# Performance work log

Measured on AMD Instinct MI355X. Metric: run time of the kernel, lower is better.

## Reference

```python
import jax, jax.numpy as jnp
import numpy as np

B, S, D, H = 2, 2048, 1024, 16
DK = D // H


def setup_inputs() -> dict:
    key = jax.random.key(0)
    ks = jax.random.split(key, 11)
    s = 1.0 / np.sqrt(D)
    inp = {
        "q": jax.random.normal(ks[0], (B, S, D), jnp.float32),
        "k": jax.random.normal(ks[1], (B, S, D), jnp.float32),
        "v": jax.random.normal(ks[2], (B, S, D), jnp.float32),
        "mask": jnp.tril(jnp.ones((S, S), jnp.int32))[None, None],  # [1,1,S,S] causal
        "wq": jax.random.normal(ks[3], (D, D), jnp.float32) * s,
        "bq": jax.random.normal(ks[4], (D,), jnp.float32) * s,
        "wk": jax.random.normal(ks[5], (D, D), jnp.float32) * s,
        "bk": jax.random.normal(ks[6], (D,), jnp.float32) * s,
        "wv": jax.random.normal(ks[7], (D, D), jnp.float32) * s,
        "bv": jax.random.normal(ks[8], (D,), jnp.float32) * s,
        "wo": jax.random.normal(ks[9], (D, D), jnp.float32) * s,
        "bo": jax.random.normal(ks[10], (D,), jnp.float32) * s,
    }
    return inp


def reference(q, k, v, mask, wq, bq, wk, bk, wv, bv, wo, bo):
    # Linear projections (torch Linear: x @ W.T + b)
    def split_heads(x):  # [B,S,D] -> [B,H,S,DK]
        return x.reshape(B, S, H, DK).transpose(0, 2, 1, 3)

    query = split_heads(q @ wq.T + bq)
    key_ = split_heads(k @ wk.T + bk)
    value = split_heads(v @ wv.T + bv)

    scale = 1.0 / jnp.sqrt(jnp.asarray(DK, q.dtype))
    scores = jnp.einsum("bhqd,bhkd->bhqk", query, key_) * scale
    scores = jnp.where(mask == 0, jnp.asarray(-1e9, scores.dtype), scores)
    attn = jax.nn.softmax(scores, axis=-1)  # dropout=0.0 -> identity
    x = jnp.einsum("bhqk,bhkd->bhqd", attn, value)
    x = x.transpose(0, 2, 1, 3).reshape(B, S, D)
    return x @ wo.T + bo
```

## Files before the change

kernel.cpp:

```cpp
#include <hip/hip_runtime.h>

typedef unsigned short u16;
typedef __bf16 bf16x8 __attribute__((ext_vector_type(8)));
typedef u16 u16x8 __attribute__((ext_vector_type(8)));
typedef float f32x4 __attribute__((ext_vector_type(4)));

constexpr size_t WQo = 12582912;
constexpr size_t WOo = 15728640;
constexpr size_t QPo = 16777216;
constexpr size_t KPo = 20971520;
constexpr size_t VTo = 25165824;
constexpr size_t OOo = 29360128;

#define GLD(g, l) __builtin_amdgcn_global_load_lds( \
    (const __attribute__((address_space(1))) void*)(g), \
    (__attribute__((address_space(3))) void*)(l), 16, 0, 0)

__device__ __forceinline__ u16 f2bf(float f) {
  unsigned u = __builtin_bit_cast(unsigned, f);
  u += 0x7fffu + ((u >> 16) & 1u);
  return (u16)(u >> 16);
}

__device__ __forceinline__ f32x4 zero4() {
  f32x4 z = {0.f, 0.f, 0.f, 0.f};
  return z;
}

__device__ __forceinline__ f32x4 mfma16(u16x8 a, u16x8 b, f32x4 c) {
  return __builtin_amdgcn_mfma_f32_16x16x32_bf16(
      __builtin_bit_cast(bf16x8, a), __builtin_bit_cast(bf16x8, b), c, 0, 0, 0);
}

__global__ __launch_bounds__(256) void cast_all(
    const float4* __restrict__ q, const float4* __restrict__ k, const float4* __restrict__ v,
    const float4* __restrict__ wq, const float4* __restrict__ wk,
    const float4* __restrict__ wv, const float4* __restrict__ wo,
    ushort4* __restrict__ dst)
{
  int i = blockIdx.x * 256 + threadIdx.x;
  constexpr int QN = 1048576;
  constexpr int WN = 262144;
  float4 val;
  if (i < QN)            val = q[i];
  else if (i < 2 * QN)   val = k[i - QN];
  else if (i < 3 * QN)   val = v[i - 2 * QN];
  else {
    int j = i - 3 * QN;
    if (j < WN)          val = wq[j];
    else if (j < 2 * WN) val = wk[j - WN];
    else if (j < 3 * WN) val = wv[j - 2 * WN];
    else                 val = wo[j - 3 * WN];
  }
  ushort4 o;
  o.x = f2bf(val.x); o.y = f2bf(val.y); o.z = f2bf(val.z); o.w = f2bf(val.w);
  dst[i] = o;
}

__device__ __forceinline__ void gemm_core(
    const u16* __restrict__ A, const u16* __restrict__ W,
    const float* __restrict__ bias, void* __restrict__ outp, int mode)
{
  constexpr int Kd = 1024;
  __shared__ u16 As[128 * 32];
  __shared__ u16 Bs[128 * 32];
  const int tid = threadIdx.x;
  const int wave = tid >> 6, lane = tid & 63;
  const int q4 = lane >> 4, l15 = lane & 15;
  const int m0 = blockIdx.y * 128, n0 = blockIdx.x * 128;
  const int wm = (wave >> 1) * 64, wn = (wave & 1) * 64;

  f32x4 acc[4][4];
#pragma unroll
  for (int i = 0; i < 4; ++i)
#pragma unroll
    for (int j = 0; j < 4; ++j) acc[i][j] = zero4();

  const int ch0 = wave * 128 + lane;
  const int ch1 = ch0 + 64;
  const int ra0 = ch0 >> 2, ka0 = (ch0 & 3) * 8;
  const int ra1 = ch1 >> 2, ka1 = (ch1 & 3) * 8;

  for (int kt = 0; kt < Kd; kt += 32) {
    GLD(A + (size_t)(m0 + ra0) * Kd + kt + ka0, As + wave * 1024);
    GLD(A + (size_t)(m0 + ra1) * Kd + kt + ka1, As + wave * 1024 + 512);
    GLD(W + (size_t)(n0 + ra0) * Kd + kt + ka0, Bs + wave * 1024);
    GLD(W + (size_t)(n0 + ra1) * Kd + kt + ka1, Bs + wave * 1024 + 512);
    __syncthreads();
    u16x8 af[4], bfv[4];
#pragma unroll
    for (int i = 0; i < 4; ++i)
      af[i] = *(const u16x8*)&As[(wm + i * 16 + l15) * 32 + q4 * 8];
#pragma unroll
    for (int j = 0; j < 4; ++j)
      bfv[j] = *(const u16x8*)&Bs[(wn + j * 16 + l15) * 32 + q4 * 8];
#pragma unroll
    for (int i = 0; i < 4; ++i)
#pragma unroll
      for (int j = 0; j < 4; ++j)
        acc[i][j] = mfma16(af[i], bfv[j], acc[i][j]);
    __syncthreads();
  }

#pragma unroll
  for (int i = 0; i < 4; ++i) {
    const int mb = m0 + wm + i * 16 + q4 * 4;
#pragma unroll
    for (int j = 0; j < 4; ++j) {
      const int col = n0 + wn + j * 16 + l15;
      const float bsv = bias[col];
#pragma unroll
      for (int r = 0; r < 4; ++r) {
        const float val = acc[i][j][r] + bsv;
        const int m = mb + r;
        if (mode == 0) {
          const int bb = m >> 11, s = m & 2047, hh = col >> 6, dk = col & 63;
          ((u16*)outp)[((size_t)(bb * 16 + hh) * 2048 + s) * 64 + dk] = f2bf(val);
        } else if (mode == 1) {
          const int bb = m >> 11, s = m & 2047, hh = col >> 6, dk = col & 63;
          ((u16*)outp)[((size_t)(bb * 16 + hh) * 64 + dk) * 2048 + s] = f2bf(val);
        } else {
          ((float*)outp)[(size_t)m * 1024 + col] = val;
        }
      }
    }
  }
}

__global__ __launch_bounds__(256) void proj_gemm(
    u16* __restrict__ ws, const float* __restrict__ bq,
    const float* __restrict__ bk, const float* __restrict__ bv)
{
  const int z = blockIdx.z;
  const u16* A = ws + (size_t)z * 4194304;
  const u16* W = ws + WQo + (size_t)z * 1048576;
  const float* bias = (z == 0) ? bq : ((z == 1) ? bk : bv);
  u16* outp = ws + QPo + (size_t)z * 4194304;
  gemm_core(A, W, bias, outp, (z == 2) ? 1 : 0);
}

__global__ __launch_bounds__(256) void out_gemm(
    const u16* __restrict__ ws, const float* __restrict__ bo, float* __restrict__ out)
{
  gemm_core(ws + OOo, ws + WOo, bo, out, 3);
}

__global__ __launch_bounds__(256) void flash_attn(u16* __restrict__ ws)
{
  constexpr int S = 2048;
  const int a = blockIdx.x;
  const int b = 31 - blockIdx.x;
  const int bh = blockIdx.y;
  const int bb = bh >> 4, h = bh & 15;
  const int tid = threadIdx.x;
  const int wave = tid >> 6, lane = tid & 63;
  const int q4 = lane >> 4, l15 = lane & 15;

  __shared__ u16 QsA[64 * 64];
  __shared__ u16 QsB[64 * 64];
  __shared__ u16 Ks[2][64 * 64];
  __shared__ u16 Vs[2][64 * 64];

  const u16* Qg = ws + QPo + (size_t)bh * S * 64;
  const u16* Kg = ws + KPo + (size_t)bh * S * 64;
  const u16* Vg = ws + VTo + (size_t)bh * 64 * S;
  u16* Og = ws + OOo;

  const int ch0 = wave * 128 + lane;
  const int ch1 = ch0 + 64;
  const int r0 = ch0 >> 3, c0 = (ch0 & 7) ^ (r0 & 7);
  const int r1 = ch1 >> 3, c1 = (ch1 & 7) ^ (r1 & 7);

  GLD(Qg + (size_t)(a * 64 + r0) * 64 + c0 * 8, QsA + wave * 1024);
  GLD(Qg + (size_t)(a * 64 + r1) * 64 + c1 * 8, QsA + wave * 1024 + 512);
  GLD(Qg + (size_t)(b * 64 + r0) * 64 + c0 * 8, QsB + wave * 1024);
  GLD(Qg + (size_t)(b * 64 + r1) * 64 + c1 * 8, QsB + wave * 1024 + 512);
  GLD(Kg + (size_t)r0 * 64 + c0 * 8, Ks[0] + wave * 1024);
  GLD(Kg + (size_t)r1 * 64 + c1 * 8, Ks[0] + wave * 1024 + 512);
  GLD(Vg + (size_t)r0 * S + c0 * 8, Vs[0] + wave * 1024);
  GLD(Vg + (size_t)r1 * S + c1 * 8, Vs[0] + wave * 1024 + 512);
  __syncthreads();

  u16x8 qfA[2], qfB[2];
  {
    const int row = wave * 16 + l15;
#pragma unroll
    for (int kk = 0; kk < 2; ++kk) {
      const int c = (kk * 4 + q4) ^ (row & 7);
      qfA[kk] = *(const u16x8*)&QsA[row * 64 + c * 8];
      qfB[kk] = *(const u16x8*)&QsB[row * 64 + c * 8];
    }
  }
  u16* Ps = QsA + wave * 1024;

  f32x4 oA[4], oB[4];
  float lA[4], lB[4];
#pragma unroll
  for (int j = 0; j < 4; ++j) { oA[j] = zero4(); oB[j] = zero4(); }
#pragma unroll
  for (int r = 0; r < 4; ++r) { lA[r] = 0.f; lB[r] = 0.f; }

  for (int kt = 0; kt <= b; ++kt) {
    const u16* Ksb = Ks[kt & 1];
    const u16* Vsb = Vs[kt & 1];
    if (kt < b) {
      const u16* Kt = Kg + (size_t)(kt + 1) * 64 * 64;
      u16* Kd = Ks[(kt + 1) & 1];
      u16* Vd = Vs[(kt + 1) & 1];
      GLD(Kt + (size_t)r0 * 64 + c0 * 8, Kd + wave * 1024);
      GLD(Kt + (size_t)r1 * 64 + c1 * 8, Kd + wave * 1024 + 512);
      GLD(Vg + (size_t)r0 * S + (kt + 1) * 64 + c0 * 8, Vd + wave * 1024);
      GLD(Vg + (size_t)r1 * S + (kt + 1) * 64 + c1 * 8, Vd + wave * 1024 + 512);
    }

    auto process = [&](const u16x8* qf, f32x4* o_acc, float* l_p, int qt, bool diag) {
      f32x4 sf[4];
#pragma unroll
      for (int j = 0; j < 4; ++j) {
        f32x4 z = zero4();
        const int row = j * 16 + l15;
#pragma unroll
        for (int kk = 0; kk < 2; ++kk) {
          const int c = (kk * 4 + q4) ^ (row & 7);
          z = mfma16(qf[kk], *(const u16x8*)&Ksb[row * 64 + c * 8], z);
        }
        sf[j] = z;
      }
      if (diag) {
        const int rowg0 = qt * 64 + wave * 16 + q4 * 4;
#pragma unroll
        for (int j = 0; j < 4; ++j) {
          const int colg = kt * 64 + j * 16 + l15;
#pragma unroll
          for (int r = 0; r < 4; ++r) {
            float val = sf[j][r] * 0.125f;
            if (colg > rowg0 + r) val = -__builtin_inff();
            sf[j][r] = __expf(val);
          }
        }
      } else {
#pragma unroll
        for (int j = 0; j < 4; ++j)
#pragma unroll
          for (int r = 0; r < 4; ++r)
            sf[j][r] = __expf(sf[j][r] * 0.125f);
      }
#pragma unroll
      for (int j = 0; j < 4; ++j)
#pragma unroll
        for (int r = 0; r < 4; ++r) l_p[r] += sf[j][r];

#pragma unroll
      for (int j = 0; j < 4; ++j)
#pragma unroll
        for (int r = 0; r < 4; ++r) {
          const int m = q4 * 4 + r;
          const int srow = j * 16 + l15;
          const int pos = m * 64 + (((srow >> 3) ^ (m & 7)) << 3) + (srow & 7);
          Ps[pos] = f2bf(sf[j][r]);
        }
      u16x8 pf[2];
#pragma unroll
      for (int kk = 0; kk < 2; ++kk) {
        const int c = (kk * 4 + q4) ^ (l15 & 7);
        pf[kk] = *(const u16x8*)&Ps[l15 * 64 + c * 8];
      }
#pragma unroll
      for (int j = 0; j < 4; ++j) {
        const int row = j * 16 + l15;
#pragma unroll
        for (int kk = 0; kk < 2; ++kk) {
          const int c = (kk * 4 + q4) ^ (row & 7);
          o_acc[j] = mfma16(pf[kk], *(const u16x8*)&Vsb[row * 64 + c * 8], o_acc[j]);
        }
      }
    };

    process(qfB, oB, lB, b, kt == b);
    if (kt <= a) process(qfA, oA, lA, a, kt == a);
    __syncthreads();
  }

#pragma unroll
  for (int off = 1; off < 16; off <<= 1)
#pragma unroll
    for (int r = 0; r < 4; ++r) {
      lA[r] += __shfl_xor(lA[r], off, 64);
      lB[r] += __shfl_xor(lB[r], off, 64);
    }

#pragma unroll
  for (int r = 0; r < 4; ++r) {
    const float invA = 1.f / lA[r];
    const float invB = 1.f / lB[r];
    const int sA = a * 64 + wave * 16 + q4 * 4 + r;
    const int sB = b * 64 + wave * 16 + q4 * 4 + r;
    const size_t baseA = ((size_t)(bb * 2048 + sA)) * 1024 + h * 64;
    const size_t baseB = ((size_t)(bb * 2048 + sB)) * 1024 + h * 64;
#pragma unroll
    for (int j = 0; j < 4; ++j) {
      Og[baseA + j * 16 + l15] = f2bf(oA[j][r] * invA);
      Og[baseB + j * 16 + l15] = f2bf(oB[j][r] * invB);
    }
  }
}

extern "C" void kernel_launch(void* const* d_in, const int* in_sizes, int n_in,
                              void* d_out, int out_size, void* d_ws, size_t ws_size,
                              hipStream_t stream)
{
  const float* q  = (const float*)d_in[0];
  const float* k  = (const float*)d_in[1];
  const float* v  = (const float*)d_in[2];
  const float* wq = (const float*)d_in[4];
  const float* bq = (const float*)d_in[5];
  const float* wk = (const float*)d_in[6];
  const float* bk = (const float*)d_in[7];
  const float* wv = (const float*)d_in[8];
  const float* bv = (const float*)d_in[9];
  const float* wo = (const float*)d_in[10];
  const float* bo = (const float*)d_in[11];
  u16* ws = (u16*)d_ws;
  float* out = (float*)d_out;

  cast_all<<<16384, 256, 0, stream>>>(
      (const float4*)q, (const float4*)k, (const float4*)v,
      (const float4*)wq, (const float4*)wk, (const float4*)wv, (const float4*)wo,
      (ushort4*)ws);
  proj_gemm<<<dim3(8, 32, 3), 256, 0, stream>>>(ws, bq, bk, bv);
  flash_attn<<<dim3(16, 32), 256, 0, stream>>>(ws);
  out_gemm<<<dim3(8, 32), 256, 0, stream>>>(ws, bo, out);
}
```

Baseline: 239.8 us.

## Deepen GEMM K-tile to 64 with XOR-swizzled LDS and smaller out-GEMM tiles

The shared GEMM core now stages a K=64 slab per iteration instead of 32, which halves the barrier pairs. It XOR-swizzles the 16-byte LDS chunks to avoid bank conflicts on fragment reads. The tile height is templated: the output projection uses 64-row tiles so it launches twice as many blocks on the device, and the V-transpose store is packed into 8-byte vector writes. The larger LDS footprint per block may reduce occupancy.

```diff
diff --git a/kernel.cpp b/kernel.cpp
--- a/kernel.cpp
+++ b/kernel.cpp
@@ -57,70 +57,92 @@
   dst[i] = o;
 }
 
+template <int TM>
 __device__ __forceinline__ void gemm_core(
     const u16* __restrict__ A, const u16* __restrict__ W,
     const float* __restrict__ bias, void* __restrict__ outp, int mode)
 {
   constexpr int Kd = 1024;
-  __shared__ u16 As[128 * 32];
-  __shared__ u16 Bs[128 * 32];
+  constexpr int BM = TM * 32;
+  constexpr int ACALLS = BM * 8 / 256;
+  __shared__ u16 As[BM * 64];
+  __shared__ u16 Bs[128 * 64];
   const int tid = threadIdx.x;
   const int wave = tid >> 6, lane = tid & 63;
   const int q4 = lane >> 4, l15 = lane & 15;
-  const int m0 = blockIdx.y * 128, n0 = blockIdx.x * 128;
-  const int wm = (wave >> 1) * 64, wn = (wave & 1) * 64;
-
-  f32x4 acc[4][4];
-#pragma unroll
-  for (int i = 0; i < 4; ++i)
+  const int m0 = blockIdx.y * BM, n0 = blockIdx.x * 128;
+  const int wm = (wave >> 1) * (TM * 16), wn = (wave & 1) * 64;
+
+  f32x4 acc[TM][4];
+#pragma unroll
+  for (int i = 0; i < TM; ++i)
 #pragma unroll
     for (int j = 0; j < 4; ++j) acc[i][j] = zero4();
 
-  const int ch0 = wave * 128 + lane;
-  const int ch1 = ch0 + 64;
-  const int ra0 = ch0 >> 2, ka0 = (ch0 & 3) * 8;
-  const int ra1 = ch1 >> 2, ka1 = (ch1 & 3) * 8;
-
-  for (int kt = 0; kt < Kd; kt += 32) {
-    GLD(A + (size_t)(m0 + ra0) * Kd + kt + ka0, As + wave * 1024);
-    GLD(A + (size_t)(m0 + ra1) * Kd + kt + ka1, As + wave * 1024 + 512);
-    GLD(W + (size_t)(n0 + ra0) * Kd + kt + ka0, Bs + wave * 1024);
-    GLD(W + (size_t)(n0 + ra1) * Kd + kt + ka1, Bs + wave * 1024 + 512);
+  for (int kt = 0; kt < Kd; kt += 64) {
+#pragma unroll
+    for (int t = 0; t < ACALLS; ++t) {
+      const int pos = t * 256 + wave * 64 + lane;
+      const int row = pos >> 3, c = (pos & 7) ^ (row & 7);
+      GLD(A + (size_t)(m0 + row) * Kd + kt + c * 8, As + t * 2048 + wave * 512);
+    }
+#pragma unroll
+    for (int t = 0; t < 4; ++t) {
+      const int pos = t * 256 + wave * 64 + lane;
+      const int row = pos >> 3, c = (pos & 7) ^ (row & 7);
+      GLD(W + (size_t)(n0 + row) * Kd + kt + c * 8, Bs + t * 2048 + wave * 512);
+    }
     __syncthreads();
-    u16x8 af[4], bfv[4];
-#pragma unroll
-    for (int i = 0; i < 4; ++i)
-      af[i] = *(const u16x8*)&As[(wm + i * 16 + l15) * 32 + q4 * 8];
-#pragma unroll
-    for (int j = 0; j < 4; ++j)
-      bfv[j] = *(const u16x8*)&Bs[(wn + j * 16 + l15) * 32 + q4 * 8];
-#pragma unroll
-    for (int i = 0; i < 4; ++i)
-#pragma unroll
-      for (int j = 0; j < 4; ++j)
-        acc[i][j] = mfma16(af[i], bfv[j], acc[i][j]);
+#pragma unroll
+    for (int h = 0; h < 2; ++h) {
+      u16x8 af[TM], bfv[4];
+#pragma unroll
+      for (int i = 0; i < TM; ++i) {
+        const int row = wm + i * 16 + l15;
+        const int p = (h * 4 + q4) ^ (row & 7);
+        af[i] = *(const u16x8*)&As[row * 64 + p * 8];
+      }
+#pragma unroll
+      for (int j = 0; j < 4; ++j) {
+        const int row = wn + j * 16 + l15;
+        const int p = (h * 4 + q4) ^ (row & 7);
+        bfv[j] = *(const u16x8*)&Bs[row * 64 + p * 8];
+      }
+#pragma unroll
+      for (int i = 0; i < TM; ++i)
+#pragma unroll
+        for (int j = 0; j < 4; ++j)
+          acc[i][j] = mfma16(af[i], bfv[j], acc[i][j]);
+    }
     __syncthreads();
   }
 
 #pragma unroll
-  for (int i = 0; i < 4; ++i) {
+  for (int i = 0; i < TM; ++i) {
     const int mb = m0 + wm + i * 16 + q4 * 4;
 #pragma unroll
     for (int j = 0; j < 4; ++j) {
       const int col = n0 + wn + j * 16 + l15;
       const float bsv = bias[col];
-#pragma unroll
-      for (int r = 0; r < 4; ++r) {
-        const float val = acc[i][j][r] + bsv;
-        const int m = mb + r;
-        if (mode == 0) {
-          const int bb = m >> 11, s = m & 2047, hh = col >> 6, dk = col & 63;
-          ((u16*)outp)[((size_t)(bb * 16 + hh) * 2048 + s) * 64 + dk] = f2bf(val);
-        } else if (mode == 1) {
-          const int bb = m >> 11, s = m & 2047, hh = col >> 6, dk = col & 63;
-          ((u16*)outp)[((size_t)(bb * 16 + hh) * 64 + dk) * 2048 + s] = f2bf(val);
-        } else {
-          ((float*)outp)[(size_t)m * 1024 + col] = val;
+      if (mode == 1) {
+        const int bb = mb >> 11, s = mb & 2047, hh = col >> 6, dk = col & 63;
+        ushort4 pk;
+        pk.x = f2bf(acc[i][j][0] + bsv);
+        pk.y = f2bf(acc[i][j][1] + bsv);
+        pk.z = f2bf(acc[i][j][2] + bsv);
+        pk.w = f2bf(acc[i][j][3] + bsv);
+        *(ushort4*)&((u16*)outp)[((size_t)(bb * 16 + hh) * 64 + dk) * 2048 + s] = pk;
+      } else {
+#pragma unroll
+        for (int r = 0; r < 4; ++r) {
+          const float val = acc[i][j][r] + bsv;
+          const int m = mb + r;
+          if (mode == 0) {
+            const int bb = m >> 11, s = m & 2047, hh = col >> 6, dk = col & 63;
+            ((u16*)outp)[((size_t)(bb * 16 + hh) * 2048 + s) * 64 + dk] = f2bf(val);
+          } else {
+            ((float*)outp)[(size_t)m * 1024 + col] = val;
+          }
         }
       }
     }
@@ -136,13 +158,13 @@
   const u16* W = ws + WQo + (size_t)z * 1048576;
   const float* bias = (z == 0) ? bq : ((z == 1) ? bk : bv);
   u16* outp = ws + QPo + (size_t)z * 4194304;
-  gemm_core(A, W, bias, outp, (z == 2) ? 1 : 0);
+  gemm_core<4>(A, W, bias, outp, (z == 2) ? 1 : 0);
 }
 
 __global__ __launch_bounds__(256) void out_gemm(
     const u16* __restrict__ ws, const float* __restrict__ bo, float* __restrict__ out)
 {
-  gemm_core(ws + OOo, ws + WOo, bo, out, 3);
+  gemm_core<2>(ws + OOo, ws + WOo, bo, out, 3);
 }
 
 __global__ __launch_bounds__(256) void flash_attn(u16* __restrict__ ws)
@@ -329,5 +351,5 @@
       (ushort4*)ws);
   proj_gemm<<<dim3(8, 32, 3), 256, 0, stream>>>(ws, bq, bk, bv);
   flash_attn<<<dim3(16, 32), 256, 0, stream>>>(ws);
-  out_gemm<<<dim3(8, 32), 256, 0, stream>>>(ws, bo, out);
-}
+  out_gemm<<<dim3(8, 64), 256, 0, stream>>>(ws, bo, out);
+}
```

New measurement: 236.6 us. Within noise of the previous version (-1.3%).
